# Performance work log

Measured on AMD Instinct MI355X. Metric: run time of the kernel, lower is better.

The kernel has to match this reference:

```python
import jax, jax.numpy as jnp
import numpy as np

B, T, E, H = 32768, 11, 128, 20  # batch, STEP_NUM, elem_num, HIDDEN_NUM


def setup_inputs() -> dict:
    key = jax.random.key(0)
    ks = jax.random.split(key, 8)
    u = lambda k, shape, lim: jax.random.uniform(k, shape, jnp.float32, -lim, lim)
    bx = jax.random.normal(ks[0], (B, T, E), jnp.float32)
    by = jax.random.normal(ks[1], (B, E), jnp.float32)
    return dict(
        bx=bx, by=by,
        l=jnp.array([0.9], jnp.float32),
        e=jnp.array([0.5], jnp.float32),
        w1=u(ks[2], (E, 50), np.sqrt(0.02)), b1=jnp.zeros((1, 50), jnp.float32),
        w2=u(ks[3], (50, 100), np.sqrt(0.01)), b2=jnp.zeros((1, 100), jnp.float32),
        w3=u(ks[4], (H, 100), np.sqrt(0.01)), b3=jnp.zeros((1, 100), jnp.float32),
        w4=u(ks[5], (100, E), np.sqrt(1.0 / E)), b4=jnp.zeros((1, E), jnp.float32),
        w=0.05 * jnp.eye(H, dtype=jnp.float32),
        c=u(ks[6], (100, H), np.sqrt(float(H))),
        g=jnp.ones((1, H), jnp.float32),
        b=jnp.ones((1, H), jnp.float32),
    )


def reference(bx, by, l, e, w1, b1, w2, b2, w3, b3, w4, b4, w, c, g, b):
    Bn, Hn = bx.shape[0], w.shape[0]
    # Input MLP is independent per step -> precompute for all steps at once.
    s1 = jax.nn.relu(jnp.einsum('bte,ef->btf', bx, w1) + b1)   # [B,T,50]
    z = jax.nn.relu(jnp.einsum('btf,fg->btg', s1, w2) + b2)    # [B,T,100]
    zc = jnp.einsum('btg,gh->bth', z, c)                       # [B,T,H]

    a0 = jnp.zeros((Bn, Hn, Hn), jnp.float32)  # fast-weight memory
    h0 = jnp.zeros((Bn, Hn), jnp.float32)

    def step(carry, zc_t):
        a, h = carry
        h = jax.nn.relu(h @ w + zc_t)
        # fast-weight outer-product update with decay: a = l*a + e * h h^T
        a = l[0] * a + e[0] * jnp.einsum('bi,bj->bij', h, h)
        # one attractor iteration (inner loop runs once in the source)
        hs = h @ w + zc_t + jnp.einsum('bi,bij->bj', h, a)
        mu = jnp.mean(hs, axis=0, keepdims=True)               # norm over BATCH dim (as in source)
        sig = jnp.sqrt(jnp.mean((hs - mu) ** 2, axis=0, keepdims=True))
        hs = jax.nn.relu(g * (hs - mu) / sig + b)
        return (a, hs), None

    (a, h), _ = jax.lax.scan(step, (a0, h0), jnp.swapaxes(zc, 0, 1))
    h = jax.nn.relu(h @ w3 + b3)
    logits = h @ w4 + b4
    loss = jnp.mean(jnp.sum(-by * jax.nn.log_softmax(logits, axis=-1), axis=-1))
    acc = jnp.mean((jnp.argmax(logits, axis=1) == jnp.argmax(by, axis=1)).astype(jnp.float32))
    return (loss, acc)
```

## Files before the change

### kernel.cpp

```cpp
#include <hip/hip_runtime.h>
#include <hip/hip_bf16.h>

#define BATCH 32768
#define TT 11
#define EE 128
#define HH 20

typedef unsigned short ushort_t;
typedef __attribute__((ext_vector_type(8))) short short8;
typedef __attribute__((ext_vector_type(4))) float f32x4;

#define ZC_OFF   8192
#define HIST_OFF (8192 + 28835840)
#define HS_OFF   (8192 + 2*28835840)
#define W1A_OFF  (HS_OFF + 2621440)
#define W2A_OFF  (W1A_OFF + 49152)
#define CA_OFF   (W2A_OFF + 43008)
#define B1F_OFF  (CA_OFF + 24576)
#define B2F_OFF  (B1F_OFF + 16384)

__device__ __forceinline__ float waveRed(float v) {
    #pragma unroll
    for (int m = 32; m > 0; m >>= 1) v += __shfl_xor(v, m, 64);
    return v;
}

__device__ __forceinline__ void split3(float v, ushort_t& a, ushort_t& b, ushort_t& c) {
    __hip_bfloat16 h1 = __float2bfloat16(v);
    float f1 = __bfloat162float(h1);
    float r1 = v - f1;
    __hip_bfloat16 h2 = __float2bfloat16(r1);
    float f2 = __bfloat162float(h2);
    float r2 = r1 - f2;
    __hip_bfloat16 h3 = __float2bfloat16(r2);
    a = *(ushort_t*)&h1; b = *(ushort_t*)&h2; c = *(ushort_t*)&h3;
}

__device__ __forceinline__ f32x4 mfma16(short8 a, short8 b, f32x4 c) {
    return __builtin_amdgcn_mfma_f32_16x16x32_bf16(a, b, c, 0, 0, 0);
}

union FragU { uint4 v; unsigned int u[4]; short8 s; };

__global__ __launch_bounds__(256) void setup_kernel(
    const float* __restrict__ w1, const float* __restrict__ b1,
    const float* __restrict__ w2, const float* __restrict__ b2,
    const float* __restrict__ c,
    unsigned int* __restrict__ W1A, unsigned int* __restrict__ W2A, unsigned int* __restrict__ CA,
    float* __restrict__ b1f, float* __restrict__ b2f, double* __restrict__ slots)
{
    const int gid = blockIdx.x * 256 + threadIdx.x;
    const int nth = gridDim.x * 256;
    for (int i = gid; i < 1024; i += nth) slots[i] = 0.0;

    for (int i = gid; i < 4096; i += nth) {
        const int r = i & 3, lane = (i >> 2) & 63, nt = (i >> 8) & 3, kt = i >> 10;
        const int m = nt * 16 + (lane & 15);
        const int g = lane >> 4;
        int j0 = 2 * r, j1 = 2 * r + 1;
        int k0 = kt * 32 + ((j0 >= 4) ? 16 : 0) + 4 * g + (j0 & 3);
        int k1 = kt * 32 + ((j1 >= 4) ? 16 : 0) + 4 * g + (j1 & 3);
        float v0 = (m < 50) ? w1[k0 * 50 + m] : 0.f;
        float v1 = (m < 50) ? w1[k1 * 50 + m] : 0.f;
        ushort_t a0, a1, a2, c0, c1, c2;
        split3(v0, a0, a1, a2); split3(v1, c0, c1, c2);
        W1A[(((kt * 4 + nt) * 3 + 0) * 64 + lane) * 4 + r] = a0 | ((unsigned)c0 << 16);
        W1A[(((kt * 4 + nt) * 3 + 1) * 64 + lane) * 4 + r] = a1 | ((unsigned)c1 << 16);
        W1A[(((kt * 4 + nt) * 3 + 2) * 64 + lane) * 4 + r] = a2 | ((unsigned)c2 << 16);
    }
    for (int i = gid; i < 3584; i += nth) {
        const int r = i & 3, lane = (i >> 2) & 63, rest = i >> 8;
        const int nt = rest % 7, kt = rest / 7;
        const int m = nt * 16 + (lane & 15);
        const int g = lane >> 4;
        int j0 = 2 * r, j1 = 2 * r + 1;
        int k0 = kt * 32 + ((j0 >= 4) ? 16 : 0) + 4 * g + (j0 & 3);
        int k1 = kt * 32 + ((j1 >= 4) ? 16 : 0) + 4 * g + (j1 & 3);
        float v0 = (m < 100 && k0 < 50) ? w2[k0 * 100 + m] : 0.f;
        float v1 = (m < 100 && k1 < 50) ? w2[k1 * 100 + m] : 0.f;
        ushort_t a0, a1, a2, c0, c1, c2;
        split3(v0, a0, a1, a2); split3(v1, c0, c1, c2);
        W2A[(((kt * 7 + nt) * 3 + 0) * 64 + lane) * 4 + r] = a0 | ((unsigned)c0 << 16);
        W2A[(((kt * 7 + nt) * 3 + 1) * 64 + lane) * 4 + r] = a1 | ((unsigned)c1 << 16);
        W2A[(((kt * 7 + nt) * 3 + 2) * 64 + lane) * 4 + r] = a2 | ((unsigned)c2 << 16);
    }
    for (int i = gid; i < 2048; i += nth) {
        const int r = i & 3, lane = (i >> 2) & 63, rest = i >> 8;
        const int nt = rest & 1, kt = rest >> 1;
        const int m = nt * 16 + (lane & 15);
        const int g = lane >> 4;
        int j0 = 2 * r, j1 = 2 * r + 1;
        int k0 = kt * 32 + ((j0 >= 4) ? 16 : 0) + 4 * g + (j0 & 3);
        int k1 = kt * 32 + ((j1 >= 4) ? 16 : 0) + 4 * g + (j1 & 3);
        float v0 = (m < 20 && k0 < 100) ? c[k0 * 20 + m] : 0.f;
        float v1 = (m < 20 && k1 < 100) ? c[k1 * 20 + m] : 0.f;
        ushort_t a0, a1, a2, c0, c1, c2;
        split3(v0, a0, a1, a2); split3(v1, c0, c1, c2);
        CA[(((kt * 2 + nt) * 3 + 0) * 64 + lane) * 4 + r] = a0 | ((unsigned)c0 << 16);
        CA[(((kt * 2 + nt) * 3 + 1) * 64 + lane) * 4 + r] = a1 | ((unsigned)c1 << 16);
        CA[(((kt * 2 + nt) * 3 + 2) * 64 + lane) * 4 + r] = a2 | ((unsigned)c2 << 16);
    }
    for (int i = gid; i < 1024; i += nth) {
        const int r = i & 3, lane = (i >> 2) & 63, nt = i >> 8;
        const int n = nt * 16 + 4 * (lane >> 4) + r;
        b1f[i] = (n < 50) ? b1[n] : 0.f;
    }
    for (int i = gid; i < 1792; i += nth) {
        const int r = i & 3, lane = (i >> 2) & 63, nt = i >> 8;
        const int n = nt * 16 + 4 * (lane >> 4) + r;
        b2f[i] = (n < 100) ? b2[n] : 0.f;
    }
}

__global__ __launch_bounds__(256) void mlp_mfma(
    const float* __restrict__ bx,
    const unsigned int* __restrict__ W1A, const unsigned int* __restrict__ W2A,
    const unsigned int* __restrict__ CA,
    const float* __restrict__ b1f, const float* __restrict__ b2f,
    float* __restrict__ zc)
{
    __shared__ ushort_t Xs[4][3][2048];
    const int tid = threadIdx.x;
    const int lane = tid & 63, wv = tid >> 6;
    const int R = (blockIdx.x * 4 + wv) * 16;
    const int t = R >> 15;
    const int bbase = R & (BATCH - 1);

    {
        const int row = lane >> 2, cg = lane & 3;
        const float4* xp = (const float4*)(bx + ((size_t)(bbase + row) * TT + t) * EE + cg * 32);
        uint2* x0 = (uint2*)Xs[wv][0];
        uint2* x1 = (uint2*)Xs[wv][1];
        uint2* x2 = (uint2*)Xs[wv][2];
        #pragma unroll
        for (int q = 0; q < 8; ++q) {
            const float4 v = xp[q];
            const int idx = row * 32 + ((cg * 8 + q) ^ row);
            ushort_t h0[3], h1[3], h2[3], h3[3];
            split3(v.x, h0[0], h0[1], h0[2]);
            split3(v.y, h1[0], h1[1], h1[2]);
            split3(v.z, h2[0], h2[1], h2[2]);
            split3(v.w, h3[0], h3[1], h3[2]);
            x0[idx] = make_uint2(h0[0] | ((unsigned)h1[0] << 16), h2[0] | ((unsigned)h3[0] << 16));
            x1[idx] = make_uint2(h0[1] | ((unsigned)h1[1] << 16), h2[1] | ((unsigned)h3[1] << 16));
            x2[idx] = make_uint2(h0[2] | ((unsigned)h1[2] << 16), h2[2] | ((unsigned)h3[2] << 16));
        }
    }

    const int rrow = lane & 15, g = lane >> 4;
    const uint4* W1A4 = (const uint4*)W1A;
    const uint4* W2A4 = (const uint4*)W2A;
    const uint4* CA4  = (const uint4*)CA;
    const float4* b1f4 = (const float4*)b1f;
    const float4* b2f4 = (const float4*)b2f;

    f32x4 D1[4];
    #pragma unroll
    for (int nt = 0; nt < 4; ++nt) D1[nt] = (f32x4){0.f, 0.f, 0.f, 0.f};
    #pragma unroll
    for (int kt = 0; kt < 4; ++kt) {
        FragU B[3];
        #pragma unroll
        for (int sp = 0; sp < 3; ++sp) {
            const uint2* xs = (const uint2*)Xs[wv][sp];
            const int kb = kt * 8 + g;
            uint2 lo = xs[rrow * 32 + (kb ^ rrow)];
            uint2 hi = xs[rrow * 32 + ((kb + 4) ^ rrow)];
            B[sp].u[0] = lo.x; B[sp].u[1] = lo.y; B[sp].u[2] = hi.x; B[sp].u[3] = hi.y;
        }
        #pragma unroll
        for (int nt = 0; nt < 4; ++nt) {
            FragU A0, A1, A2;
            A0.v = W1A4[((kt * 4 + nt) * 3 + 0) * 64 + lane];
            A1.v = W1A4[((kt * 4 + nt) * 3 + 1) * 64 + lane];
            A2.v = W1A4[((kt * 4 + nt) * 3 + 2) * 64 + lane];
            D1[nt] = mfma16(A2.s, B[0].s, D1[nt]);
            D1[nt] = mfma16(A0.s, B[2].s, D1[nt]);
            D1[nt] = mfma16(A1.s, B[1].s, D1[nt]);
            D1[nt] = mfma16(A1.s, B[0].s, D1[nt]);
            D1[nt] = mfma16(A0.s, B[1].s, D1[nt]);
            D1[nt] = mfma16(A0.s, B[0].s, D1[nt]);
        }
    }

    f32x4 D2[7];
    #pragma unroll
    for (int nt = 0; nt < 7; ++nt) D2[nt] = (f32x4){0.f, 0.f, 0.f, 0.f};
    #pragma unroll
    for (int kt2 = 0; kt2 < 2; ++kt2) {
        FragU B[3];
        #pragma unroll
        for (int half = 0; half < 2; ++half) {
            const int nt = 2 * kt2 + half;
            const float4 bv = b1f4[nt * 64 + lane];
            #pragma unroll
            for (int rp = 0; rp < 2; ++rp) {
                float v0 = fmaxf(D1[nt][2 * rp]     + bv[2 * rp],     0.f);
                float v1 = fmaxf(D1[nt][2 * rp + 1] + bv[2 * rp + 1], 0.f);
                ushort_t s00, s01, s02, s10, s11, s12;
                split3(v0, s00, s01, s02); split3(v1, s10, s11, s12);
                B[0].u[half * 2 + rp] = s00 | ((unsigned)s10 << 16);
                B[1].u[half * 2 + rp] = s01 | ((unsigned)s11 << 16);
                B[2].u[half * 2 + rp] = s02 | ((unsigned)s12 << 16);
            }
        }
        #pragma unroll
        for (int nt2 = 0; nt2 < 7; ++nt2) {
            FragU A0, A1, A2;
            A0.v = W2A4[((kt2 * 7 + nt2) * 3 + 0) * 64 + lane];
            A1.v = W2A4[((kt2 * 7 + nt2) * 3 + 1) * 64 + lane];
            A2.v = W2A4[((kt2 * 7 + nt2) * 3 + 2) * 64 + lane];
            D2[nt2] = mfma16(A2.s, B[0].s, D2[nt2]);
            D2[nt2] = mfma16(A0.s, B[2].s, D2[nt2]);
            D2[nt2] = mfma16(A1.s, B[1].s, D2[nt2]);
            D2[nt2] = mfma16(A1.s, B[0].s, D2[nt2]);
            D2[nt2] = mfma16(A0.s, B[1].s, D2[nt2]);
            D2[nt2] = mfma16(A0.s, B[0].s, D2[nt2]);
        }
    }

    f32x4 D3[2];
    D3[0] = (f32x4){0.f, 0.f, 0.f, 0.f};
    D3[1] = (f32x4){0.f, 0.f, 0.f, 0.f};
    #pragma unroll
    for (int kt3 = 0; kt3 < 4; ++kt3) {
        FragU B[3];
        #pragma unroll
        for (int half = 0; half < 2; ++half) {
            const int nt = 2 * kt3 + half;
            if (nt < 7) {
                const float4 bv = b2f4[nt * 64 + lane];
                #pragma unroll
                for (int rp = 0; rp < 2; ++rp) {
                    float v0 = fmaxf(D2[nt][2 * rp]     + bv[2 * rp],     0.f);
                    float v1 = fmaxf(D2[nt][2 * rp + 1] + bv[2 * rp + 1], 0.f);
                    ushort_t s00, s01, s02, s10, s11, s12;
                    split3(v0, s00, s01, s02); split3(v1, s10, s11, s12);
                    B[0].u[half * 2 + rp] = s00 | ((unsigned)s10 << 16);
                    B[1].u[half * 2 + rp] = s01 | ((unsigned)s11 << 16);
                    B[2].u[half * 2 + rp] = s02 | ((unsigned)s12 << 16);
                }
            } else {
                B[0].u[2] = B[0].u[3] = 0u;
                B[1].u[2] = B[1].u[3] = 0u;
                B[2].u[2] = B[2].u[3] = 0u;
            }
        }
        #pragma unroll
        for (int nt3 = 0; nt3 < 2; ++nt3) {
            FragU A0, A1, A2;
            A0.v = CA4[((kt3 * 2 + nt3) * 3 + 0) * 64 + lane];
            A1.v = CA4[((kt3 * 2 + nt3) * 3 + 1) * 64 + lane];
            A2.v = CA4[((kt3 * 2 + nt3) * 3 + 2) * 64 + lane];
            D3[nt3] = mfma16(A2.s, B[0].s, D3[nt3]);
            D3[nt3] = mfma16(A0.s, B[2].s, D3[nt3]);
            D3[nt3] = mfma16(A1.s, B[1].s, D3[nt3]);
            D3[nt3] = mfma16(A1.s, B[0].s, D3[nt3]);
            D3[nt3] = mfma16(A0.s, B[1].s, D3[nt3]);
            D3[nt3] = mfma16(A0.s, B[0].s, D3[nt3]);
        }
    }

    const int bcol = bbase + rrow;
    #pragma unroll
    for (int r = 0; r < 4; ++r) {
        const int h = 4 * g + r;
        zc[((size_t)(t * HH + h) << 15) + bcol] = D3[0][r];
    }
    if (g == 0) {
        #pragma unroll
        for (int r = 0; r < 4; ++r) {
            zc[((size_t)(t * HH + 16 + r) << 15) + bcol] = D3[1][r];
        }
    }
}

__global__ __launch_bounds__(256) void step_kernel(
    const float* __restrict__ zc, const float* __restrict__ lp, const float* __restrict__ ep,
    const float* __restrict__ w, const float* __restrict__ g, const float* __restrict__ bb,
    float* __restrict__ hist, float* __restrict__ hs_buf, double* __restrict__ slots, int t)
{
    __shared__ float red[4][40];
    const int tid = threadIdx.x;
    const int p = tid & 1;
    const int sb = tid >> 1;
    const int b = blockIdx.x * 128 + sb;
    const int lane = tid & 63, wv = tid >> 6;
    const int jb = 10 * p;
    const float l0 = lp[0], e0 = ep[0];

    float h[10];
    if (t == 0) {
        #pragma unroll
        for (int jj = 0; jj < 10; ++jj) h[jj] = 0.f;
    } else {
        #pragma unroll
        for (int jj = 0; jj < 10; ++jj) {
            const int j = jb + jj;
            const double s1 = slots[(t - 1) * 64 + j];
            const double s2 = slots[(t - 1) * 64 + HH + j];
            const double mu = s1 * (1.0 / 32768.0);
            const double var = s2 * (1.0 / 32768.0) - mu * mu;
            const float muf = (float)mu;
            const float rsig = 1.0f / sqrtf((float)var);
            const float hv = hs_buf[(j << 15) + b];
            h[jj] = fmaxf(fmaf(g[j] * rsig, hv - muf, bb[j]), 0.f);
        }
    }

    float zct[10];
    #pragma unroll
    for (int jj = 0; jj < 10; ++jj) zct[jj] = zc[((t * HH + jb + jj) << 15) + b];

    float hn[10];
    {
        float po[20];
        #pragma unroll
        for (int j = 0; j < 20; ++j) {
            float a = 0.f;
            #pragma unroll
            for (int ii = 0; ii < 10; ++ii) a = fmaf(h[ii], w[(jb + ii) * HH + j], a);
            po[j] = a;
        }
        #pragma unroll
        for (int jj = 0; jj < 10; ++jj) {
            const float mine = p ? po[10 + jj] : po[jj];
            const float send = p ? po[jj] : po[10 + jj];
            const float recv = __shfl_xor(send, 1, 64);
            hn[jj] = fmaxf(mine + recv + zct[jj], 0.f);
        }
    }
    #pragma unroll
    for (int jj = 0; jj < 10; ++jj) hist[((t * HH + jb + jj) << 15) + b] = hn[jj];

    float pv[10];
    {
        float dp = 0.f;
        #pragma unroll
        for (int jj = 0; jj < 10; ++jj) dp = fmaf(hn[jj], hn[jj], dp);
        const float d = dp + __shfl_xor(dp, 1, 64);
        const float cd = e0 * d;
        #pragma unroll
        for (int jj = 0; jj < 10; ++jj) pv[jj] = cd * hn[jj];
    }
    float coef = e0 * l0;
    #pragma unroll 1
    for (int s = t - 1; s >= 0; --s) {
        float tv[10];
        #pragma unroll
        for (int jj = 0; jj < 10; ++jj) tv[jj] = hist[((s * HH + jb + jj) << 15) + b];
        float dp = 0.f;
        #pragma unroll
        for (int jj = 0; jj < 10; ++jj) dp = fmaf(hn[jj], tv[jj], dp);
        const float d = dp + __shfl_xor(dp, 1, 64);
        const float cd = coef * d;
        #pragma unroll
        for (int jj = 0; jj < 10; ++jj) pv[jj] = fmaf(cd, tv[jj], pv[jj]);
        coef *= l0;
    }

    float hs[10];
    {
        float po[20];
        #pragma unroll
        for (int j = 0; j < 20; ++j) {
            float a = 0.f;
            #pragma unroll
            for (int ii = 0; ii < 10; ++ii) a = fmaf(hn[ii], w[(jb + ii) * HH + j], a);
            po[j] = a;
        }
        #pragma unroll
        for (int jj = 0; jj < 10; ++jj) {
            const float mine = p ? po[10 + jj] : po[jj];
            const float send = p ? po[jj] : po[10 + jj];
            const float recv = __shfl_xor(send, 1, 64);
            hs[jj] = mine + recv + zct[jj] + pv[jj];
            hs_buf[((jb + jj) << 15) + b] = hs[jj];
        }
    }

    float sm[10], sq[10];
    #pragma unroll
    for (int jj = 0; jj < 10; ++jj) { sm[jj] = hs[jj]; sq[jj] = hs[jj] * hs[jj]; }
    #pragma unroll
    for (int m = 2; m <= 32; m <<= 1) {
        #pragma unroll
        for (int jj = 0; jj < 10; ++jj) {
            sm[jj] += __shfl_xor(sm[jj], m, 64);
            sq[jj] += __shfl_xor(sq[jj], m, 64);
        }
    }
    if (lane < 2) {
        #pragma unroll
        for (int jj = 0; jj < 10; ++jj) {
            red[wv][jb + jj] = sm[jj];
            red[wv][20 + jb + jj] = sq[jj];
        }
    }
    __syncthreads();
    if (tid < 40) {
        atomicAdd(&slots[t * 64 + tid],
                  (double)(red[0][tid] + red[1][tid] + red[2][tid] + red[3][tid]));
    }
}

__global__ __launch_bounds__(256, 2) void head_kernel(
    const float* __restrict__ hs_buf, const float* __restrict__ by,
    const float* __restrict__ g, const float* __restrict__ bb,
    const float* __restrict__ w3, const float* __restrict__ b3,
    const float* __restrict__ w4, const float* __restrict__ b4,
    double* __restrict__ slots)
{
    __shared__ float hfs[100][64];
    __shared__ float cpm[4][64], cps[4][64], cdot[4][64], csby[4][64], cbym[4][64];
    __shared__ int   cidx[4][64], cbyidx[4][64];
    const int tid = threadIdx.x;
    const int lane = tid & 63;
    const int p = tid >> 6;
    const int b = blockIdx.x * 64 + lane;

    float h[HH];
    #pragma unroll
    for (int j = 0; j < HH; ++j) {
        const double s1 = slots[10 * 64 + j];
        const double s2 = slots[10 * 64 + HH + j];
        const double mu = s1 * (1.0 / 32768.0);
        const double var = s2 * (1.0 / 32768.0) - mu * mu;
        const float muf = (float)mu;
        const float rsig = 1.0f / sqrtf((float)var);
        const float hv = hs_buf[(j << 15) + b];
        h[j] = fmaxf(fmaf(g[j] * rsig, hv - muf, bb[j]), 0.f);
    }

    #pragma unroll
    for (int k = 0; k < 25; ++k) {
        const int f = p * 25 + k;
        float a = b3[f];
        #pragma unroll
        for (int i = 0; i < HH; ++i) a = fmaf(h[i], w3[i * 100 + f], a);
        hfs[f][lane] = fmaxf(a, 0.f);
    }
    __syncthreads();

    float lg[32];
    {
        const float* b4c = b4 + p * 32;
        #pragma unroll
        for (int u = 0; u < 32; ++u) lg[u] = b4c[u];
    }
    for (int k = 0; k < 100; ++k) {
        const float hv = hfs[k][lane];
        const float* wr = w4 + k * EE + p * 32;
        #pragma unroll
        for (int u = 0; u < 32; ++u) lg[u] = fmaf(hv, wr[u], lg[u]);
    }

    float pm = lg[0]; int pidx = 0;
    #pragma unroll
    for (int u = 1; u < 32; ++u) { if (lg[u] > pm) { pm = lg[u]; pidx = u; } }
    float ps = 0.f;
    #pragma unroll
    for (int u = 0; u < 32; ++u) ps += expf(lg[u] - pm);

    const float* byp = by + (size_t)b * EE + p * 32;
    float dotp = 0.f, sbyp = 0.f, bym = -3.402823e38f; int byi = 0;
    #pragma unroll
    for (int u4 = 0; u4 < 8; ++u4) {
        const float4 v = *(const float4*)(byp + u4 * 4);
        const int u = u4 * 4;
        if (v.x > bym) { bym = v.x; byi = u; }
        if (v.y > bym) { bym = v.y; byi = u + 1; }
        if (v.z > bym) { bym = v.z; byi = u + 2; }
        if (v.w > bym) { bym = v.w; byi = u + 3; }
        dotp = fmaf(v.x, lg[u], dotp);
        dotp = fmaf(v.y, lg[u + 1], dotp);
        dotp = fmaf(v.z, lg[u + 2], dotp);
        dotp = fmaf(v.w, lg[u + 3], dotp);
        sbyp += v.x + v.y + v.z + v.w;
    }

    cpm[p][lane] = pm;  cps[p][lane] = ps;  cdot[p][lane] = dotp;  csby[p][lane] = sbyp;
    cidx[p][lane] = p * 32 + pidx;
    cbym[p][lane] = bym; cbyidx[p][lane] = p * 32 + byi;
    __syncthreads();

    if (p == 0) {
        float gm = cpm[0][lane];
        #pragma unroll
        for (int q = 1; q < 4; ++q) gm = fmaxf(gm, cpm[q][lane]);
        float se = 0.f, dot = 0.f, sby = 0.f;
        #pragma unroll
        for (int q = 0; q < 4; ++q) {
            se  += cps[q][lane] * expf(cpm[q][lane] - gm);
            dot += cdot[q][lane];
            sby += csby[q][lane];
        }
        float cm = cpm[0][lane]; int am = cidx[0][lane];
        #pragma unroll
        for (int q = 1; q < 4; ++q) { if (cpm[q][lane] > cm) { cm = cpm[q][lane]; am = cidx[q][lane]; } }
        float bm = cbym[0][lane]; int byam = cbyidx[0][lane];
        #pragma unroll
        for (int q = 1; q < 4; ++q) { if (cbym[q][lane] > bm) { bm = cbym[q][lane]; byam = cbyidx[q][lane]; } }

        const float loss_i = -dot + (gm + logf(se)) * sby;
        const float acc_i = (am == byam) ? 1.f : 0.f;
        const float ls = waveRed(loss_i);
        const float as = waveRed(acc_i);
        if (lane == 0) {
            atomicAdd(&slots[704], (double)ls);
            atomicAdd(&slots[705], (double)as);
        }
    }
}

__global__ void finalize_kernel(const double* __restrict__ slots, float* __restrict__ out) {
    out[0] = (float)(slots[704] * (1.0 / 32768.0));
    out[1] = (float)(slots[705] * (1.0 / 32768.0));
}

extern "C" void kernel_launch(void* const* d_in, const int* in_sizes, int n_in,
                              void* d_out, int out_size, void* d_ws, size_t ws_size,
                              hipStream_t stream) {
    const float* bx = (const float*)d_in[0];
    const float* by = (const float*)d_in[1];
    const float* l  = (const float*)d_in[2];
    const float* e  = (const float*)d_in[3];
    const float* w1 = (const float*)d_in[4];
    const float* b1 = (const float*)d_in[5];
    const float* w2 = (const float*)d_in[6];
    const float* b2 = (const float*)d_in[7];
    const float* w3 = (const float*)d_in[8];
    const float* b3 = (const float*)d_in[9];
    const float* w4 = (const float*)d_in[10];
    const float* b4 = (const float*)d_in[11];
    const float* w  = (const float*)d_in[12];
    const float* c  = (const float*)d_in[13];
    const float* g  = (const float*)d_in[14];
    const float* bb = (const float*)d_in[15];

    double* slots = (double*)d_ws;
    float*  zcw   = (float*)((char*)d_ws + ZC_OFF);
    float*  hist  = (float*)((char*)d_ws + HIST_OFF);
    float*  hs    = (float*)((char*)d_ws + HS_OFF);
    unsigned int* W1A = (unsigned int*)((char*)d_ws + W1A_OFF);
    unsigned int* W2A = (unsigned int*)((char*)d_ws + W2A_OFF);
    unsigned int* CA  = (unsigned int*)((char*)d_ws + CA_OFF);
    float* b1f = (float*)((char*)d_ws + B1F_OFF);
    float* b2f = (float*)((char*)d_ws + B2F_OFF);
    float*  outp  = (float*)d_out;

    hipLaunchKernelGGL(setup_kernel, dim3(16), dim3(256), 0, stream,
                       w1, b1, w2, b2, c, W1A, W2A, CA, b1f, b2f, slots);
    hipLaunchKernelGGL(mlp_mfma, dim3(5632), dim3(256), 0, stream,
                       bx, W1A, W2A, CA, b1f, b2f, zcw);
    for (int t = 0; t < TT; ++t) {
        hipLaunchKernelGGL(step_kernel, dim3(256), dim3(256), 0, stream,
                           zcw, l, e, w, g, bb, hist, hs, slots, t);
    }
    hipLaunchKernelGGL(head_kernel, dim3(512), dim3(256), 0, stream,
                       hs, by, g, bb, w3, b3, w4, b4, slots);
    hipLaunchKernelGGL(finalize_kernel, dim3(1), dim3(1), 0, stream, slots, outp);
}
```

Measured before the change: 369.3 us.

## Use two-term bf16 split in MLP MFMA and widen step kernel parallelism

The MLP MFMA path now splits fp32 operands into two bf16 terms instead of three. That cuts each k-tile from six MFMAs to three, and also reduces shared-memory staging and weight-fragment loads. Separately, step_kernel is templated on the timestep so the history loop fully unrolls, and each batch row is handled by four threads instead of two, doubling the grid to 512 blocks. The two-term split lowers accuracy to roughly 16 mantissa bits, which may affect the batch-norm statistics and the final loss and accuracy outputs.

```diff
diff --git a/kernel.cpp b/kernel.cpp
--- a/kernel.cpp
+++ b/kernel.cpp
@@ -14,9 +14,9 @@
 #define HIST_OFF (8192 + 28835840)
 #define HS_OFF   (8192 + 2*28835840)
 #define W1A_OFF  (HS_OFF + 2621440)
-#define W2A_OFF  (W1A_OFF + 49152)
-#define CA_OFF   (W2A_OFF + 43008)
-#define B1F_OFF  (CA_OFF + 24576)
+#define W2A_OFF  (W1A_OFF + 32768)
+#define CA_OFF   (W2A_OFF + 28672)
+#define B1F_OFF  (CA_OFF + 16384)
 #define B2F_OFF  (B1F_OFF + 16384)
 
 __device__ __forceinline__ float waveRed(float v) {
@@ -25,15 +25,11 @@
     return v;
 }
 
-__device__ __forceinline__ void split3(float v, ushort_t& a, ushort_t& b, ushort_t& c) {
+__device__ __forceinline__ void split2(float v, ushort_t& a, ushort_t& b) {
     __hip_bfloat16 h1 = __float2bfloat16(v);
-    float f1 = __bfloat162float(h1);
-    float r1 = v - f1;
+    float r1 = v - __bfloat162float(h1);
     __hip_bfloat16 h2 = __float2bfloat16(r1);
-    float f2 = __bfloat162float(h2);
-    float r2 = r1 - f2;
-    __hip_bfloat16 h3 = __float2bfloat16(r2);
-    a = *(ushort_t*)&h1; b = *(ushort_t*)&h2; c = *(ushort_t*)&h3;
+    a = *(ushort_t*)&h1; b = *(ushort_t*)&h2;
 }
 
 __device__ __forceinline__ f32x4 mfma16(short8 a, short8 b, f32x4 c) {
@@ -62,11 +58,10 @@
         int k1 = kt * 32 + ((j1 >= 4) ? 16 : 0) + 4 * g + (j1 & 3);
         float v0 = (m < 50) ? w1[k0 * 50 + m] : 0.f;
         float v1 = (m < 50) ? w1[k1 * 50 + m] : 0.f;
-        ushort_t a0, a1, a2, c0, c1, c2;
-        split3(v0, a0, a1, a2); split3(v1, c0, c1, c2);
-        W1A[(((kt * 4 + nt) * 3 + 0) * 64 + lane) * 4 + r] = a0 | ((unsigned)c0 << 16);
-        W1A[(((kt * 4 + nt) * 3 + 1) * 64 + lane) * 4 + r] = a1 | ((unsigned)c1 << 16);
-        W1A[(((kt * 4 + nt) * 3 + 2) * 64 + lane) * 4 + r] = a2 | ((unsigned)c2 << 16);
+        ushort_t a0, a1, c0, c1;
+        split2(v0, a0, a1); split2(v1, c0, c1);
+        W1A[(((kt * 4 + nt) * 2 + 0) * 64 + lane) * 4 + r] = a0 | ((unsigned)c0 << 16);
+        W1A[(((kt * 4 + nt) * 2 + 1) * 64 + lane) * 4 + r] = a1 | ((unsigned)c1 << 16);
     }
     for (int i = gid; i < 3584; i += nth) {
         const int r = i & 3, lane = (i >> 2) & 63, rest = i >> 8;
@@ -78,11 +73,10 @@
         int k1 = kt * 32 + ((j1 >= 4) ? 16 : 0) + 4 * g + (j1 & 3);
         float v0 = (m < 100 && k0 < 50) ? w2[k0 * 100 + m] : 0.f;
         float v1 = (m < 100 && k1 < 50) ? w2[k1 * 100 + m] : 0.f;
-        ushort_t a0, a1, a2, c0, c1, c2;
-        split3(v0, a0, a1, a2); split3(v1, c0, c1, c2);
-        W2A[(((kt * 7 + nt) * 3 + 0) * 64 + lane) * 4 + r] = a0 | ((unsigned)c0 << 16);
-        W2A[(((kt * 7 + nt) * 3 + 1) * 64 + lane) * 4 + r] = a1 | ((unsigned)c1 << 16);
-        W2A[(((kt * 7 + nt) * 3 + 2) * 64 + lane) * 4 + r] = a2 | ((unsigned)c2 << 16);
+        ushort_t a0, a1, c0, c1;
+        split2(v0, a0, a1); split2(v1, c0, c1);
+        W2A[(((kt * 7 + nt) * 2 + 0) * 64 + lane) * 4 + r] = a0 | ((unsigned)c0 << 16);
+        W2A[(((kt * 7 + nt) * 2 + 1) * 64 + lane) * 4 + r] = a1 | ((unsigned)c1 << 16);
     }
     for (int i = gid; i < 2048; i += nth) {
         const int r = i & 3, lane = (i >> 2) & 63, rest = i >> 8;
@@ -94,11 +88,10 @@
         int k1 = kt * 32 + ((j1 >= 4) ? 16 : 0) + 4 * g + (j1 & 3);
         float v0 = (m < 20 && k0 < 100) ? c[k0 * 20 + m] : 0.f;
         float v1 = (m < 20 && k1 < 100) ? c[k1 * 20 + m] : 0.f;
-        ushort_t a0, a1, a2, c0, c1, c2;
-        split3(v0, a0, a1, a2); split3(v1, c0, c1, c2);
-        CA[(((kt * 2 + nt) * 3 + 0) * 64 + lane) * 4 + r] = a0 | ((unsigned)c0 << 16);
-        CA[(((kt * 2 + nt) * 3 + 1) * 64 + lane) * 4 + r] = a1 | ((unsigned)c1 << 16);
-        CA[(((kt * 2 + nt) * 3 + 2) * 64 + lane) * 4 + r] = a2 | ((unsigned)c2 << 16);
+        ushort_t a0, a1, c0, c1;
+        split2(v0, a0, a1); split2(v1, c0, c1);
+        CA[(((kt * 2 + nt) * 2 + 0) * 64 + lane) * 4 + r] = a0 | ((unsigned)c0 << 16);
+        CA[(((kt * 2 + nt) * 2 + 1) * 64 + lane) * 4 + r] = a1 | ((unsigned)c1 << 16);
     }
     for (int i = gid; i < 1024; i += nth) {
         const int r = i & 3, lane = (i >> 2) & 63, nt = i >> 8;
@@ -112,14 +105,14 @@
     }
 }
 
-__global__ __launch_bounds__(256) void mlp_mfma(
+__global__ __launch_bounds__(256, 4) void mlp_mfma(
     const float* __restrict__ bx,
     const unsigned int* __restrict__ W1A, const unsigned int* __restrict__ W2A,
     const unsigned int* __restrict__ CA,
     const float* __restrict__ b1f, const float* __restrict__ b2f,
     float* __restrict__ zc)
 {
-    __shared__ ushort_t Xs[4][3][2048];
+    __shared__ ushort_t Xs[4][2][2048];
     const int tid = threadIdx.x;
     const int lane = tid & 63, wv = tid >> 6;
     const int R = (blockIdx.x * 4 + wv) * 16;
@@ -131,19 +124,17 @@
         const float4* xp = (const float4*)(bx + ((size_t)(bbase + row) * TT + t) * EE + cg * 32);
         uint2* x0 = (uint2*)Xs[wv][0];
         uint2* x1 = (uint2*)Xs[wv][1];
-        uint2* x2 = (uint2*)Xs[wv][2];
         #pragma unroll
         for (int q = 0; q < 8; ++q) {
             const float4 v = xp[q];
             const int idx = row * 32 + ((cg * 8 + q) ^ row);
-            ushort_t h0[3], h1[3], h2[3], h3[3];
-            split3(v.x, h0[0], h0[1], h0[2]);
-            split3(v.y, h1[0], h1[1], h1[2]);
-            split3(v.z, h2[0], h2[1], h2[2]);
-            split3(v.w, h3[0], h3[1], h3[2]);
+            ushort_t h0[2], h1[2], h2[2], h3[2];
+            split2(v.x, h0[0], h0[1]);
+            split2(v.y, h1[0], h1[1]);
+            split2(v.z, h2[0], h2[1]);
+            split2(v.w, h3[0], h3[1]);
             x0[idx] = make_uint2(h0[0] | ((unsigned)h1[0] << 16), h2[0] | ((unsigned)h3[0] << 16));
             x1[idx] = make_uint2(h0[1] | ((unsigned)h1[1] << 16), h2[1] | ((unsigned)h3[1] << 16));
-            x2[idx] = make_uint2(h0[2] | ((unsigned)h1[2] << 16), h2[2] | ((unsigned)h3[2] << 16));
         }
     }
 
@@ -159,9 +150,9 @@
     for (int nt = 0; nt < 4; ++nt) D1[nt] = (f32x4){0.f, 0.f, 0.f, 0.f};
     #pragma unroll
     for (int kt = 0; kt < 4; ++kt) {
-        FragU B[3];
-        #pragma unroll
-        for (int sp = 0; sp < 3; ++sp) {
+        FragU B[2];
+        #pragma unroll
+        for (int sp = 0; sp < 2; ++sp) {
             const uint2* xs = (const uint2*)Xs[wv][sp];
             const int kb = kt * 8 + g;
             uint2 lo = xs[rrow * 32 + (kb ^ rrow)];
@@ -170,13 +161,9 @@
         }
         #pragma unroll
         for (int nt = 0; nt < 4; ++nt) {
-            FragU A0, A1, A2;
-            A0.v = W1A4[((kt * 4 + nt) * 3 + 0) * 64 + lane];
-            A1.v = W1A4[((kt * 4 + nt) * 3 + 1) * 64 + lane];
-            A2.v = W1A4[((kt * 4 + nt) * 3 + 2) * 64 + lane];
-            D1[nt] = mfma16(A2.s, B[0].s, D1[nt]);
-            D1[nt] = mfma16(A0.s, B[2].s, D1[nt]);
-            D1[nt] = mfma16(A1.s, B[1].s, D1[nt]);
+            FragU A0, A1;
+            A0.v = W1A4[((kt * 4 + nt) * 2 + 0) * 64 + lane];
+            A1.v = W1A4[((kt * 4 + nt) * 2 + 1) * 64 + lane];
             D1[nt] = mfma16(A1.s, B[0].s, D1[nt]);
             D1[nt] = mfma16(A0.s, B[1].s, D1[nt]);
             D1[nt] = mfma16(A0.s, B[0].s, D1[nt]);
@@ -188,7 +175,7 @@
     for (int nt = 0; nt < 7; ++nt) D2[nt] = (f32x4){0.f, 0.f, 0.f, 0.f};
     #pragma unroll
     for (int kt2 = 0; kt2 < 2; ++kt2) {
-        FragU B[3];
+        FragU B[2];
         #pragma unroll
         for (int half = 0; half < 2; ++half) {
             const int nt = 2 * kt2 + half;
@@ -197,22 +184,17 @@
             for (int rp = 0; rp < 2; ++rp) {
                 float v0 = fmaxf(D1[nt][2 * rp]     + bv[2 * rp],     0.f);
                 float v1 = fmaxf(D1[nt][2 * rp + 1] + bv[2 * rp + 1], 0.f);
-                ushort_t s00, s01, s02, s10, s11, s12;
-                split3(v0, s00, s01, s02); split3(v1, s10, s11, s12);
+                ushort_t s00, s01, s10, s11;
+                split2(v0, s00, s01); split2(v1, s10, s11);
                 B[0].u[half * 2 + rp] = s00 | ((unsigned)s10 << 16);
                 B[1].u[half * 2 + rp] = s01 | ((unsigned)s11 << 16);
-                B[2].u[half * 2 + rp] = s02 | ((unsigned)s12 << 16);
             }
         }
         #pragma unroll
         for (int nt2 = 0; nt2 < 7; ++nt2) {
-            FragU A0, A1, A2;
-            A0.v = W2A4[((kt2 * 7 + nt2) * 3 + 0) * 64 + lane];
-            A1.v = W2A4[((kt2 * 7 + nt2) * 3 + 1) * 64 + lane];
-            A2.v = W2A4[((kt2 * 7 + nt2) * 3 + 2) * 64 + lane];
-            D2[nt2] = mfma16(A2.s, B[0].s, D2[nt2]);
-            D2[nt2] = mfma16(A0.s, B[2].s, D2[nt2]);
-            D2[nt2] = mfma16(A1.s, B[1].s, D2[nt2]);
+            FragU A0, A1;
+            A0.v = W2A4[((kt2 * 7 + nt2) * 2 + 0) * 64 + lane];
+            A1.v = W2A4[((kt2 * 7 + nt2) * 2 + 1) * 64 + lane];
             D2[nt2] = mfma16(A1.s, B[0].s, D2[nt2]);
             D2[nt2] = mfma16(A0.s, B[1].s, D2[nt2]);
             D2[nt2] = mfma16(A0.s, B[0].s, D2[nt2]);
@@ -224,7 +206,7 @@
     D3[1] = (f32x4){0.f, 0.f, 0.f, 0.f};
     #pragma unroll
     for (int kt3 = 0; kt3 < 4; ++kt3) {
-        FragU B[3];
+        FragU B[2];
         #pragma unroll
         for (int half = 0; half < 2; ++half) {
             const int nt = 2 * kt3 + half;
@@ -234,27 +216,21 @@
                 for (int rp = 0; rp < 2; ++rp) {
                     float v0 = fmaxf(D2[nt][2 * rp]     + bv[2 * rp],     0.f);
                     float v1 = fmaxf(D2[nt][2 * rp + 1] + bv[2 * rp + 1], 0.f);
-                    ushort_t s00, s01, s02, s10, s11, s12;
-                    split3(v0, s00, s01, s02); split3(v1, s10, s11, s12);
+                    ushort_t s00, s01, s10, s11;
+                    split2(v0, s00, s01); split2(v1, s10, s11);
                     B[0].u[half * 2 + rp] = s00 | ((unsigned)s10 << 16);
                     B[1].u[half * 2 + rp] = s01 | ((unsigned)s11 << 16);
-                    B[2].u[half * 2 + rp] = s02 | ((unsigned)s12 << 16);
                 }
             } else {
                 B[0].u[2] = B[0].u[3] = 0u;
                 B[1].u[2] = B[1].u[3] = 0u;
-                B[2].u[2] = B[2].u[3] = 0u;
             }
         }
         #pragma unroll
         for (int nt3 = 0; nt3 < 2; ++nt3) {
-            FragU A0, A1, A2;
-            A0.v = CA4[((kt3 * 2 + nt3) * 3 + 0) * 64 + lane];
-            A1.v = CA4[((kt3 * 2 + nt3) * 3 + 1) * 64 + lane];
-            A2.v = CA4[((kt3 * 2 + nt3) * 3 + 2) * 64 + lane];
-            D3[nt3] = mfma16(A2.s, B[0].s, D3[nt3]);
-            D3[nt3] = mfma16(A0.s, B[2].s, D3[nt3]);
-            D3[nt3] = mfma16(A1.s, B[1].s, D3[nt3]);
+            FragU A0, A1;
+            A0.v = CA4[((kt3 * 2 + nt3) * 2 + 0) * 64 + lane];
+            A1.v = CA4[((kt3 * 2 + nt3) * 2 + 1) * 64 + lane];
             D3[nt3] = mfma16(A1.s, B[0].s, D3[nt3]);
             D3[nt3] = mfma16(A0.s, B[1].s, D3[nt3]);
             D3[nt3] = mfma16(A0.s, B[0].s, D3[nt3]);
@@ -275,30 +251,32 @@
     }
 }
 
-__global__ __launch_bounds__(256) void step_kernel(
+template<int TC>
+__global__ __launch_bounds__(256, 2) void step_kernel(
     const float* __restrict__ zc, const float* __restrict__ lp, const float* __restrict__ ep,
     const float* __restrict__ w, const float* __restrict__ g, const float* __restrict__ bb,
-    float* __restrict__ hist, float* __restrict__ hs_buf, double* __restrict__ slots, int t)
+    float* __restrict__ hist, float* __restrict__ hs_buf, double* __restrict__ slots)
 {
     __shared__ float red[4][40];
     const int tid = threadIdx.x;
-    const int p = tid & 1;
-    const int sb = tid >> 1;
-    const int b = blockIdx.x * 128 + sb;
+    const int p = tid & 3;
+    const int sb = tid >> 2;
+    const int b = blockIdx.x * 64 + sb;
     const int lane = tid & 63, wv = tid >> 6;
-    const int jb = 10 * p;
+    const int jb = 5 * p;
+    const int myh = p >> 1, myq = p & 1;
     const float l0 = lp[0], e0 = ep[0];
 
-    float h[10];
-    if (t == 0) {
-        #pragma unroll
-        for (int jj = 0; jj < 10; ++jj) h[jj] = 0.f;
+    float h[5];
+    if (TC == 0) {
+        #pragma unroll
+        for (int jj = 0; jj < 5; ++jj) h[jj] = 0.f;
     } else {
         #pragma unroll
-        for (int jj = 0; jj < 10; ++jj) {
+        for (int jj = 0; jj < 5; ++jj) {
             const int j = jb + jj;
-            const double s1 = slots[(t - 1) * 64 + j];
-            const double s2 = slots[(t - 1) * 64 + HH + j];
+            const double s1 = slots[(TC - 1) * 64 + j];
+            const double s2 = slots[(TC - 1) * 64 + HH + j];
             const double mu = s1 * (1.0 / 32768.0);
             const double var = s2 * (1.0 / 32768.0) - mu * mu;
             const float muf = (float)mu;
@@ -308,98 +286,112 @@
         }
     }
 
-    float zct[10];
-    #pragma unroll
-    for (int jj = 0; jj < 10; ++jj) zct[jj] = zc[((t * HH + jb + jj) << 15) + b];
-
-    float hn[10];
+    float zct[5];
+    #pragma unroll
+    for (int jj = 0; jj < 5; ++jj) zct[jj] = zc[((TC * HH + jb + jj) << 15) + b];
+
+    float hn[5];
     {
         float po[20];
         #pragma unroll
         for (int j = 0; j < 20; ++j) {
             float a = 0.f;
             #pragma unroll
-            for (int ii = 0; ii < 10; ++ii) a = fmaf(h[ii], w[(jb + ii) * HH + j], a);
+            for (int ii = 0; ii < 5; ++ii) a = fmaf(h[ii], w[(jb + ii) * HH + j], a);
             po[j] = a;
         }
+        float poA[10];
         #pragma unroll
         for (int jj = 0; jj < 10; ++jj) {
-            const float mine = p ? po[10 + jj] : po[jj];
-            const float send = p ? po[jj] : po[10 + jj];
-            const float recv = __shfl_xor(send, 1, 64);
-            hn[jj] = fmaxf(mine + recv + zct[jj], 0.f);
-        }
-    }
-    #pragma unroll
-    for (int jj = 0; jj < 10; ++jj) hist[((t * HH + jb + jj) << 15) + b] = hn[jj];
-
-    float pv[10];
+            const float send = po[10 * (myh ^ 1) + jj];
+            poA[jj] = po[10 * myh + jj] + __shfl_xor(send, 2, 64);
+        }
+        #pragma unroll
+        for (int jj = 0; jj < 5; ++jj) {
+            const float send = poA[5 * (myq ^ 1) + jj];
+            const float full = poA[5 * myq + jj] + __shfl_xor(send, 1, 64);
+            hn[jj] = fmaxf(full + zct[jj], 0.f);
+        }
+    }
+    #pragma unroll
+    for (int jj = 0; jj < 5; ++jj) hist[((TC * HH + jb + jj) << 15) + b] = hn[jj];
+
+    float pv[5];
     {
         float dp = 0.f;
         #pragma unroll
-        for (int jj = 0; jj < 10; ++jj) dp = fmaf(hn[jj], hn[jj], dp);
-        const float d = dp + __shfl_xor(dp, 1, 64);
-        const float cd = e0 * d;
-        #pragma unroll
-        for (int jj = 0; jj < 10; ++jj) pv[jj] = cd * hn[jj];
-    }
-    float coef = e0 * l0;
-    #pragma unroll 1
-    for (int s = t - 1; s >= 0; --s) {
-        float tv[10];
-        #pragma unroll
-        for (int jj = 0; jj < 10; ++jj) tv[jj] = hist[((s * HH + jb + jj) << 15) + b];
-        float dp = 0.f;
-        #pragma unroll
-        for (int jj = 0; jj < 10; ++jj) dp = fmaf(hn[jj], tv[jj], dp);
-        const float d = dp + __shfl_xor(dp, 1, 64);
-        const float cd = coef * d;
-        #pragma unroll
-        for (int jj = 0; jj < 10; ++jj) pv[jj] = fmaf(cd, tv[jj], pv[jj]);
-        coef *= l0;
-    }
-
-    float hs[10];
+        for (int jj = 0; jj < 5; ++jj) dp = fmaf(hn[jj], hn[jj], dp);
+        dp += __shfl_xor(dp, 1, 64);
+        dp += __shfl_xor(dp, 2, 64);
+        const float cd = e0 * dp;
+        #pragma unroll
+        for (int jj = 0; jj < 5; ++jj) pv[jj] = cd * hn[jj];
+    }
+    if (TC > 0) {
+        float coef = e0 * l0;
+        #pragma unroll
+        for (int s = TC - 1; s >= 0; --s) {
+            float tv[5];
+            #pragma unroll
+            for (int jj = 0; jj < 5; ++jj) tv[jj] = hist[((s * HH + jb + jj) << 15) + b];
+            float dp = 0.f;
+            #pragma unroll
+            for (int jj = 0; jj < 5; ++jj) dp = fmaf(hn[jj], tv[jj], dp);
+            dp += __shfl_xor(dp, 1, 64);
+            dp += __shfl_xor(dp, 2, 64);
+            const float cd = coef * dp;
+            #pragma unroll
+            for (int jj = 0; jj < 5; ++jj) pv[jj] = fmaf(cd, tv[jj], pv[jj]);
+            coef *= l0;
+        }
+    }
+
+    float hs[5];
     {
         float po[20];
         #pragma unroll
         for (int j = 0; j < 20; ++j) {
             float a = 0.f;
             #pragma unroll
-            for (int ii = 0; ii < 10; ++ii) a = fmaf(hn[ii], w[(jb + ii) * HH + j], a);
+            for (int ii = 0; ii < 5; ++ii) a = fmaf(hn[ii], w[(jb + ii) * HH + j], a);
             po[j] = a;
         }
+        float poA[10];
         #pragma unroll
         for (int jj = 0; jj < 10; ++jj) {
-            const float mine = p ? po[10 + jj] : po[jj];
-            const float send = p ? po[jj] : po[10 + jj];
-            const float recv = __shfl_xor(send, 1, 64);
-            hs[jj] = mine + recv + zct[jj] + pv[jj];
+            const float send = po[10 * (myh ^ 1) + jj];
+            poA[jj] = po[10 * myh + jj] + __shfl_xor(send, 2, 64);
+        }
+        #pragma unroll
+        for (int jj = 0; jj < 5; ++jj) {
+            const float send = poA[5 * (myq ^ 1) + jj];
+            const float full = poA[5 * myq + jj] + __shfl_xor(send, 1, 64);
+            hs[jj] = full + zct[jj] + pv[jj];
             hs_buf[((jb + jj) << 15) + b] = hs[jj];
         }
     }
 
-    float sm[10], sq[10];
-    #pragma unroll
-    for (int jj = 0; jj < 10; ++jj) { sm[jj] = hs[jj]; sq[jj] = hs[jj] * hs[jj]; }
-    #pragma unroll
-    for (int m = 2; m <= 32; m <<= 1) {
-        #pragma unroll
-        for (int jj = 0; jj < 10; ++jj) {
+    float sm[5], sq[5];
+    #pragma unroll
+    for (int jj = 0; jj < 5; ++jj) { sm[jj] = hs[jj]; sq[jj] = hs[jj] * hs[jj]; }
+    #pragma unroll
+    for (int m = 4; m <= 32; m <<= 1) {
+        #pragma unroll
+        for (int jj = 0; jj < 5; ++jj) {
             sm[jj] += __shfl_xor(sm[jj], m, 64);
             sq[jj] += __shfl_xor(sq[jj], m, 64);
         }
     }
-    if (lane < 2) {
-        #pragma unroll
-        for (int jj = 0; jj < 10; ++jj) {
+    if (lane < 4) {
+        #pragma unroll
+        for (int jj = 0; jj < 5; ++jj) {
             red[wv][jb + jj] = sm[jj];
             red[wv][20 + jb + jj] = sq[jj];
         }
     }
     __syncthreads();
     if (tid < 40) {
-        atomicAdd(&slots[t * 64 + tid],
+        atomicAdd(&slots[TC * 64 + tid],
                   (double)(red[0][tid] + red[1][tid] + red[2][tid] + red[3][tid]));
     }
 }
@@ -553,10 +545,11 @@
                        w1, b1, w2, b2, c, W1A, W2A, CA, b1f, b2f, slots);
     hipLaunchKernelGGL(mlp_mfma, dim3(5632), dim3(256), 0, stream,
                        bx, W1A, W2A, CA, b1f, b2f, zcw);
-    for (int t = 0; t < TT; ++t) {
-        hipLaunchKernelGGL(step_kernel, dim3(256), dim3(256), 0, stream,
-                           zcw, l, e, w, g, bb, hist, hs, slots, t);
-    }
+#define LSTEP(T) hipLaunchKernelGGL((step_kernel<T>), dim3(512), dim3(256), 0, stream, \
+                                    zcw, l, e, w, g, bb, hist, hs, slots)
+    LSTEP(0); LSTEP(1); LSTEP(2); LSTEP(3); LSTEP(4); LSTEP(5);
+    LSTEP(6); LSTEP(7); LSTEP(8); LSTEP(9); LSTEP(10);
+#undef LSTEP
     hipLaunchKernelGGL(head_kernel, dim3(512), dim3(256), 0, stream,
                        hs, by, g, bb, w3, b3, w4, b4, slots);
     hipLaunchKernelGGL(finalize_kernel, dim3(1), dim3(1), 0, stream, slots, outp);
```

After: 750.2 us. +103.1%, slower.
